# Kernel tuning notes

Hardware: AMD Instinct MI355X
Metric: run time of the kernel (lower is better)

## Reference

```python
import jax, jax.numpy as jnp
import numpy as np

B, T, C = 8, 1024, 768
H, D = 12, 64

def setup_inputs() -> dict:
    key = jax.random.key(0)
    ks = jax.random.split(key, 6)
    s = 0.02
    return {
        "x": jax.random.normal(ks[0], (B, T, C), dtype=jnp.float32),
        "Wq": jax.random.normal(ks[1], (H, C, D), dtype=jnp.float32) * s,
        "Wk": jax.random.normal(ks[2], (H, C, D), dtype=jnp.float32) * s,
        "Wv": jax.random.normal(ks[3], (H, C, D), dtype=jnp.float32) * s,
        "Wproj": jax.random.normal(ks[4], (C, C), dtype=jnp.float32) * s,
        "bproj": jnp.zeros((C,), dtype=jnp.float32),
    }

def reference(x, Wq, Wk, Wv, Wproj, bproj):
    # per-head projections, vectorized over heads: [B,H,T,D]
    q = jnp.einsum('btc,hcd->bhtd', x, Wq)
    k = jnp.einsum('btc,hcd->bhtd', x, Wk)
    v = jnp.einsum('btc,hcd->bhtd', x, Wv)
    scale = 1.0 / jnp.sqrt(jnp.asarray(q.shape[-1], q.dtype))
    scores = jnp.einsum('bhtd,bhsd->bhts', q, k) * scale  # [B,H,T,T]
    attn = jax.nn.softmax(scores, axis=-1)
    out = jnp.einsum('bhts,bhsd->bhtd', attn, v)          # [B,H,T,D]
    # concat heads along last dim -> [B,T,H*D]
    out = out.transpose(0, 2, 1, 3).reshape(x.shape[0], x.shape[1], -1)
    return out @ Wproj + bproj
```

## Files before the change

kernel.cpp:

```cpp
#include <hip/hip_runtime.h>
#include <hip/hip_bf16.h>

using u16 = unsigned short;

typedef __attribute__((ext_vector_type(8))) short bf16x8;
typedef __attribute__((ext_vector_type(4))) float f32x4;
typedef __attribute__((ext_vector_type(16))) float f32x16;

#define B_ 8
#define T_ 1024
#define C_ 768
#define H_ 12
#define D_ 64

typedef const void __attribute__((address_space(1))) gv_t;
typedef void __attribute__((address_space(3))) lv_t;

__device__ __forceinline__ void gload_lds16(const void* g, void* l) {
  __builtin_amdgcn_global_load_lds((gv_t*)g, (lv_t*)l, 16, 0, 0);
}

__device__ __forceinline__ u16 f2b(float f) {
  union { float f; unsigned u; } a; a.f = f;
  unsigned r = a.u + 0x7FFFu + ((a.u >> 16) & 1u);
  return (u16)(r >> 16);
}

__device__ __forceinline__ unsigned cvtpk_bf16(float lo, float hi) {
  unsigned r;
  asm("v_cvt_pk_bf16_f32 %0, %1, %2" : "=v"(r) : "v"(lo), "v"(hi));
  return r;
}
__device__ __forceinline__ void plane32_swap(unsigned &a, unsigned &b) {
  asm volatile("v_permlane32_swap_b32 %0, %1" : "+v"(a), "+v"(b));
}

__global__ __launch_bounds__(256) void cast_x(
    const float* __restrict__ in, u16* __restrict__ out)
{
  int i = (blockIdx.x * 256 + threadIdx.x) * 8;
  float4 a = *(const float4*)(in + i);
  float4 b = *(const float4*)(in + i + 4);
  union { bf16x8 v; u16 s[8]; } o;
  o.s[0] = f2b(a.x); o.s[1] = f2b(a.y); o.s[2] = f2b(a.z); o.s[3] = f2b(a.w);
  o.s[4] = f2b(b.x); o.s[5] = f2b(b.y); o.s[6] = f2b(b.z); o.s[7] = f2b(b.w);
  *(bf16x8*)(out + i) = o.v;
}

__global__ __launch_bounds__(256) void prep_weights(
    const float* __restrict__ Wq, const float* __restrict__ Wk,
    const float* __restrict__ Wv, const float* __restrict__ Wp,
    u16* __restrict__ Wqkvt, u16* __restrict__ Wpt)
{
  int idx = blockIdx.x * 256 + threadIdx.x;
  int p = idx / 589824;
  int r = idx - p * 589824;
  int n = r / 768, c = r - n * 768;
  if (p < 3) {
    const float* W = (p == 0) ? Wq : ((p == 1) ? Wk : Wv);
    int h = n >> 6, d = n & 63;
    Wqkvt[idx] = f2b(W[(size_t)h * (C_ * D_) + (size_t)c * D_ + d]);
  } else {
    Wpt[r] = f2b(Wp[(size_t)c * 768 + n]);
  }
}

#define GEMM_MAINLOOP(APTR, BPTR, KDIM)                                          \
  for (int k0 = 0; k0 < (KDIM); k0 += 64) {                                      \
    _Pragma("unroll")                                                            \
    for (int q = 0; q < 4; ++q) {                                                \
      int db = q * 4096 + t * 16;                                                \
      int row = db >> 7;                                                         \
      int cb = (db ^ ((row & 7) << 4)) & 127;                                    \
      gload_lds16((const char*)(APTR) + ((size_t)(m0 + row) * (KDIM) + k0) * 2 + cb, \
                  (char*)As + db);                                               \
      gload_lds16((const char*)(BPTR) + ((size_t)(n0 + row) * (KDIM) + k0) * 2 + cb, \
                  (char*)Bs + db);                                               \
    }                                                                            \
    asm volatile("s_waitcnt vmcnt(0)" ::: "memory");                             \
    __syncthreads();                                                             \
    _Pragma("unroll")                                                            \
    for (int kq = 0; kq < 2; ++kq) {                                             \
      bf16x8 af[4], bfr[4];                                                      \
      _Pragma("unroll")                                                          \
      for (int i = 0; i < 4; ++i) {                                              \
        int ra = wr + i * 16 + lr;                                               \
        int Ua = ra * 128 + kq * 64 + hc;                                        \
        af[i] = *(const bf16x8*)((const char*)As + (Ua ^ ((ra & 7) << 4)));      \
        int rb = wc + i * 16 + lr;                                               \
        int Ub = rb * 128 + kq * 64 + hc;                                        \
        bfr[i] = *(const bf16x8*)((const char*)Bs + (Ub ^ ((rb & 7) << 4)));     \
      }                                                                          \
      _Pragma("unroll")                                                          \
      for (int i = 0; i < 4; ++i)                                                \
        _Pragma("unroll")                                                        \
        for (int j = 0; j < 4; ++j)                                              \
          acc[i][j] = __builtin_amdgcn_mfma_f32_16x16x32_bf16(af[i], bfr[j],     \
                                                              acc[i][j], 0, 0, 0); \
    }                                                                            \
    __syncthreads();                                                             \
  }

__global__ __launch_bounds__(256) void gemm_qkv(
    const u16* __restrict__ X, const u16* __restrict__ Wt,
    u16* __restrict__ Qw, u16* __restrict__ Kw, u16* __restrict__ Vt)
{
  __shared__ __align__(16) u16 As[128 * 64];
  __shared__ __align__(16) u16 Bs[128 * 64];
  const int t = threadIdx.x;
  const int l = t & 63, w = t >> 6;
  const int lr = l & 15;
  const int hc = (l >> 4) * 16;
  const int m0 = blockIdx.x * 128;
  const int n0 = blockIdx.y * 128;
  const int wr = (w >> 1) * 64, wc = (w & 1) * 64;

  f32x4 acc[4][4] = {};
  GEMM_MAINLOOP(X, Wt, 768)

  #pragma unroll
  for (int j = 0; j < 4; ++j) {
    int col_g = n0 + wc + j * 16 + lr;
    int p = (col_g >= 1536) ? 2 : ((col_g >= 768) ? 1 : 0);
    int rr = col_g - p * 768;
    int h = rr >> 6, d = rr & 63;
    #pragma unroll
    for (int i = 0; i < 4; ++i) {
      int rg0 = m0 + wr + i * 16 + ((l >> 4) << 2);
      int b = rg0 >> 10, tt = rg0 & 1023;
      if (p == 0) {
        size_t base = (((size_t)b * H_ + h) * T_ + tt) * D_ + d;
        #pragma unroll
        for (int r = 0; r < 4; ++r)
          Qw[base + (size_t)r * D_] = f2b(acc[i][j][r] * 0.18033688f);
      } else if (p == 1) {
        size_t base = (((size_t)b * H_ + h) * T_ + tt) * D_ + d;
        #pragma unroll
        for (int r = 0; r < 4; ++r) Kw[base + (size_t)r * D_] = f2b(acc[i][j][r]);
      } else {
        unsigned long long pk =
            (unsigned long long)f2b(acc[i][j][0]) |
            ((unsigned long long)f2b(acc[i][j][1]) << 16) |
            ((unsigned long long)f2b(acc[i][j][2]) << 32) |
            ((unsigned long long)f2b(acc[i][j][3]) << 48);
        *reinterpret_cast<unsigned long long*>(
            &Vt[(((size_t)b * H_ + h) * D_ + d) * T_ + tt]) = pk;
      }
    }
  }
}

__global__ __launch_bounds__(256) void gemm_proj(
    const u16* __restrict__ A, const u16* __restrict__ Wt,
    const float* __restrict__ bias, float* __restrict__ O)
{
  __shared__ __align__(16) u16 As[128 * 64];
  __shared__ __align__(16) u16 Bs[128 * 64];
  const int t = threadIdx.x;
  const int l = t & 63, w = t >> 6;
  const int lr = l & 15;
  const int hc = (l >> 4) * 16;
  const int m0 = blockIdx.x * 128;
  const int n0 = blockIdx.y * 128;
  const int wr = (w >> 1) * 64, wc = (w & 1) * 64;

  f32x4 acc[4][4] = {};
  GEMM_MAINLOOP(A, Wt, 768)

  #pragma unroll
  for (int j = 0; j < 4; ++j) {
    int col_g = n0 + wc + j * 16 + lr;
    float bb = bias[col_g];
    #pragma unroll
    for (int i = 0; i < 4; ++i) {
      int rg0 = m0 + wr + i * 16 + ((l >> 4) << 2);
      #pragma unroll
      for (int r = 0; r < 4; ++r)
        O[(size_t)(rg0 + r) * C_ + col_g] = acc[i][j][r] + bb;
    }
  }
}

__global__ __launch_bounds__(256) void attn_fwd(
    const u16* __restrict__ Qw, const u16* __restrict__ Kw,
    const u16* __restrict__ VT, u16* __restrict__ AO)
{
  __shared__ __align__(16) u16 Ks[2][64 * 64];
  __shared__ __align__(16) u16 Vs[2][64 * 64];
  const int t = threadIdx.x, w = t >> 6, l = t & 63;
  const int lq = l & 31, lh = l >> 5;

  const int bid = blockIdx.x;
  const int bh = (bid & 7) * 12 + ((bid >> 3) >> 3);
  const int qt = (bid >> 3) & 7;
  const int b = bh / H_, h = bh - b * H_;
  const u16* Qh = Qw + (size_t)bh * (T_ * D_);
  const u16* Kh = Kw + (size_t)bh * (T_ * D_);
  const u16* Vh = VT + (size_t)bh * (D_ * T_);
  const int q0w = qt * 128 + w * 32;
  const int qrow = q0w + lq;

  bf16x8 qf[4];
  #pragma unroll
  for (int ks = 0; ks < 4; ++ks)
    qf[ks] = *(const bf16x8*)(Qh + (size_t)qrow * D_ + lh * 8 + ks * 16);

  f32x16 oA = {}, oB = {};
  float mrun = -1e30f, lrun = 0.f;

  const int db0 = t * 16, db1 = 4096 + t * 16;
  const int row0 = db0 >> 7, row1 = db1 >> 7;
  const int o20 = db0 & 127, o21 = db1 & 127;
  const int dsw0 = db0 ^ ((row0 & 7) << 4);
  const int dsw1 = db1 ^ ((row1 & 7) << 4);

  bf16x8 rk0, rk1, rv0, rv1;
  rk0 = *(const bf16x8*)((const char*)(Kh + (size_t)row0 * D_) + o20);
  rk1 = *(const bf16x8*)((const char*)(Kh + (size_t)row1 * D_) + o21);
  rv0 = *(const bf16x8*)((const char*)(Vh + (size_t)row0 * T_) + o20);
  rv1 = *(const bf16x8*)((const char*)(Vh + (size_t)row1 * T_) + o21);

  for (int kt_i = 0; kt_i < 16; ++kt_i) {
    const int cur = kt_i & 1;
    *(bf16x8*)((char*)Ks[cur] + dsw0) = rk0;
    *(bf16x8*)((char*)Ks[cur] + dsw1) = rk1;
    *(bf16x8*)((char*)Vs[cur] + dsw0) = rv0;
    *(bf16x8*)((char*)Vs[cur] + dsw1) = rv1;
    __syncthreads();

    if (kt_i < 15) {
      int kn = (kt_i + 1) * 64;
      rk0 = *(const bf16x8*)((const char*)(Kh + (size_t)(kn + row0) * D_) + o20);
      rk1 = *(const bf16x8*)((const char*)(Kh + (size_t)(kn + row1) * D_) + o21);
      rv0 = *(const bf16x8*)((const char*)(Vh + (size_t)row0 * T_ + kn) + o20);
      rv1 = *(const bf16x8*)((const char*)(Vh + (size_t)row1 * T_ + kn) + o21);
    }

    f32x16 sA = {}, sB = {};
    #pragma unroll
    for (int kvh = 0; kvh < 2; ++kvh) {
      bf16x8 ka[4];
      #pragma unroll
      for (int ks = 0; ks < 4; ++ks) {
        int row = lq + 32 * kvh;
        int U = row * 128 + ks * 32 + lh * 16;
        ka[ks] = *(const bf16x8*)((const char*)Ks[cur] + (U ^ ((row & 7) << 4)));
      }
      if (kvh == 0) {
        #pragma unroll
        for (int ks = 0; ks < 4; ++ks)
          sA = __builtin_amdgcn_mfma_f32_32x32x16_bf16(ka[ks], qf[ks], sA, 0, 0, 0);
      } else {
        #pragma unroll
        for (int ks = 0; ks < 4; ++ks)
          sB = __builtin_amdgcn_mfma_f32_32x32x16_bf16(ka[ks], qf[ks], sB, 0, 0, 0);
      }
    }

    float red[32];
    #pragma unroll
    for (int r = 0; r < 16; ++r) { red[r] = sA[r]; red[16 + r] = sB[r]; }
    #pragma unroll
    for (int stp = 16; stp > 0; stp >>= 1)
      #pragma unroll
      for (int r = 0; r < stp; ++r) red[r] = fmaxf(red[r], red[r + stp]);
    float mx = fmaxf(red[0], __shfl_xor(red[0], 32));
    float nm = fmaxf(mrun, mx);
    float alpha = exp2f(mrun - nm);
    mrun = nm;
    #pragma unroll
    for (int r = 0; r < 16; ++r) {
      sA[r] = exp2f(sA[r] - nm);
      sB[r] = exp2f(sB[r] - nm);
    }
    #pragma unroll
    for (int r = 0; r < 16; ++r) { red[r] = sA[r]; red[16 + r] = sB[r]; }
    #pragma unroll
    for (int stp = 16; stp > 0; stp >>= 1)
      #pragma unroll
      for (int r = 0; r < stp; ++r) red[r] += red[r + stp];
    float rs = red[0] + __shfl_xor(red[0], 32);
    lrun = lrun * alpha + rs;

    bf16x8 pb[4];
    #pragma unroll
    for (int ks = 0; ks < 4; ++ks) {
      f32x16& S = (ks < 2) ? sA : sB;
      const int g = (ks & 1) * 8;
      unsigned a0 = cvtpk_bf16(S[g + 0], S[g + 1]);
      unsigned a1 = cvtpk_bf16(S[g + 2], S[g + 3]);
      unsigned b0 = cvtpk_bf16(S[g + 4], S[g + 5]);
      unsigned b1 = cvtpk_bf16(S[g + 6], S[g + 7]);
      plane32_swap(a0, b0);
      plane32_swap(a1, b1);
      union { unsigned wd[4]; bf16x8 v; } u;
      u.wd[0] = a0; u.wd[1] = a1; u.wd[2] = b0; u.wd[3] = b1;
      pb[ks] = u.v;
    }

    #pragma unroll
    for (int r = 0; r < 16; ++r) { oA[r] *= alpha; oB[r] *= alpha; }

    #pragma unroll
    for (int dh = 0; dh < 2; ++dh) {
      bf16x8 va[4];
      #pragma unroll
      for (int ks = 0; ks < 4; ++ks) {
        int row = lq + 32 * dh;
        int U = row * 128 + ks * 32 + lh * 16;
        va[ks] = *(const bf16x8*)((const char*)Vs[cur] + (U ^ ((row & 7) << 4)));
      }
      if (dh == 0) {
        #pragma unroll
        for (int ks = 0; ks < 4; ++ks)
          oA = __builtin_amdgcn_mfma_f32_32x32x16_bf16(va[ks], pb[ks], oA, 0, 0, 0);
      } else {
        #pragma unroll
        for (int ks = 0; ks < 4; ++ks)
          oB = __builtin_amdgcn_mfma_f32_32x32x16_bf16(va[ks], pb[ks], oB, 0, 0, 0);
      }
    }
  }

  float inv = 1.0f / lrun;
  size_t base = ((size_t)b * T_ + qrow) * C_ + h * D_;
  #pragma unroll
  for (int dh = 0; dh < 2; ++dh) {
    const f32x16& OO = dh ? oB : oA;
    #pragma unroll
    for (int g = 0; g < 4; ++g) {
      int d0 = 8 * g + 4 * lh + 32 * dh;
      unsigned long long pk =
          (unsigned long long)f2b(OO[4 * g + 0] * inv) |
          ((unsigned long long)f2b(OO[4 * g + 1] * inv) << 16) |
          ((unsigned long long)f2b(OO[4 * g + 2] * inv) << 32) |
          ((unsigned long long)f2b(OO[4 * g + 3] * inv) << 48);
      *reinterpret_cast<unsigned long long*>(&AO[base + d0]) = pk;
    }
  }
}

extern "C" void kernel_launch(void* const* d_in, const int* in_sizes, int n_in,
                              void* d_out, int out_size, void* d_ws, size_t ws_size,
                              hipStream_t stream) {
  (void)in_sizes; (void)n_in; (void)out_size;
  const float* x     = (const float*)d_in[0];
  const float* Wq    = (const float*)d_in[1];
  const float* Wk    = (const float*)d_in[2];
  const float* Wv    = (const float*)d_in[3];
  const float* Wproj = (const float*)d_in[4];
  const float* bproj = (const float*)d_in[5];

  const size_t NEEDED = 55050240;
  if (ws_size < NEEDED) return;

  char* ws = (char*)d_ws;
  u16* Wpt   = (u16*)(ws);
  u16* Qw    = (u16*)(ws + 1179648);
  u16* Kw    = (u16*)(ws + 13762560);
  u16* Vt    = (u16*)(ws + 26345472);
  u16* Xb    = (u16*)(ws + 38928384);
  u16* AO    = (u16*)(ws + 38928384);
  u16* Wqkvt = (u16*)(ws + 51511296);

  cast_x<<<dim3(3072), dim3(256), 0, stream>>>(x, Xb);
  prep_weights<<<dim3(9216), dim3(256), 0, stream>>>(Wq, Wk, Wv, Wproj, Wqkvt, Wpt);
  gemm_qkv<<<dim3(64, 18), dim3(256), 0, stream>>>(Xb, Wqkvt, Qw, Kw, Vt);
  attn_fwd<<<dim3(768), dim3(256), 0, stream>>>(Qw, Kw, Vt, AO);
  gemm_proj<<<dim3(64, 6), dim3(256), 0, stream>>>(AO, Wpt, bproj, (float*)d_out);
}
```

Baseline: 151.9 us.

## Fuse prep kernels, async LDS loads in attention, lazy softmax rescale

Merges the x cast and weight-prep kernels into a single launch to save one kernel launch. In attention, K/V tiles now go straight to LDS through global_load_lds and are prefetched into the other buffer, replacing the register-staged copy. The online softmax first combines sA and sB element-wise to shorten the max/sum reductions, and rescales the running max and output only when the new max exceeds the old one by more than 8 (log2 units), skipping that multiply most of the time. The lazy rescale keeps results exact in principle but lets exp2 values grow up to 2^8 before renormalising, so bf16 P values carry a larger range.

```diff
diff --git a/kernel.cpp b/kernel.cpp
--- a/kernel.cpp
+++ b/kernel.cpp
@@ -35,33 +35,33 @@
   asm volatile("v_permlane32_swap_b32 %0, %1" : "+v"(a), "+v"(b));
 }
 
-__global__ __launch_bounds__(256) void cast_x(
-    const float* __restrict__ in, u16* __restrict__ out)
-{
-  int i = (blockIdx.x * 256 + threadIdx.x) * 8;
-  float4 a = *(const float4*)(in + i);
-  float4 b = *(const float4*)(in + i + 4);
-  union { bf16x8 v; u16 s[8]; } o;
-  o.s[0] = f2b(a.x); o.s[1] = f2b(a.y); o.s[2] = f2b(a.z); o.s[3] = f2b(a.w);
-  o.s[4] = f2b(b.x); o.s[5] = f2b(b.y); o.s[6] = f2b(b.z); o.s[7] = f2b(b.w);
-  *(bf16x8*)(out + i) = o.v;
-}
-
-__global__ __launch_bounds__(256) void prep_weights(
+__global__ __launch_bounds__(256) void prep_all(
+    const float* __restrict__ x,
     const float* __restrict__ Wq, const float* __restrict__ Wk,
     const float* __restrict__ Wv, const float* __restrict__ Wp,
-    u16* __restrict__ Wqkvt, u16* __restrict__ Wpt)
+    u16* __restrict__ Xb, u16* __restrict__ Wqkvt, u16* __restrict__ Wpt)
 {
-  int idx = blockIdx.x * 256 + threadIdx.x;
-  int p = idx / 589824;
-  int r = idx - p * 589824;
-  int n = r / 768, c = r - n * 768;
-  if (p < 3) {
-    const float* W = (p == 0) ? Wq : ((p == 1) ? Wk : Wv);
-    int h = n >> 6, d = n & 63;
-    Wqkvt[idx] = f2b(W[(size_t)h * (C_ * D_) + (size_t)c * D_ + d]);
+  int bb = blockIdx.x;
+  if (bb < 3072) {
+    int i = (bb * 256 + threadIdx.x) * 8;
+    float4 a = *(const float4*)(x + i);
+    float4 b = *(const float4*)(x + i + 4);
+    union { bf16x8 v; u16 s[8]; } o;
+    o.s[0] = f2b(a.x); o.s[1] = f2b(a.y); o.s[2] = f2b(a.z); o.s[3] = f2b(a.w);
+    o.s[4] = f2b(b.x); o.s[5] = f2b(b.y); o.s[6] = f2b(b.z); o.s[7] = f2b(b.w);
+    *(bf16x8*)(Xb + i) = o.v;
   } else {
-    Wpt[r] = f2b(Wp[(size_t)c * 768 + n]);
+    int idx = (bb - 3072) * 256 + threadIdx.x;
+    int p = idx / 589824;
+    int r = idx - p * 589824;
+    int n = r / 768, c = r - n * 768;
+    if (p < 3) {
+      const float* W = (p == 0) ? Wq : ((p == 1) ? Wk : Wv);
+      int h = n >> 6, d = n & 63;
+      Wqkvt[idx] = f2b(W[(size_t)h * (C_ * D_) + (size_t)c * D_ + d]);
+    } else {
+      Wpt[r] = f2b(Wp[(size_t)c * 768 + n]);
+    }
   }
 }
 
@@ -195,8 +195,8 @@
   const int qt = (bid >> 3) & 7;
   const int b = bh / H_, h = bh - b * H_;
   const u16* Qh = Qw + (size_t)bh * (T_ * D_);
-  const u16* Kh = Kw + (size_t)bh * (T_ * D_);
-  const u16* Vh = VT + (size_t)bh * (D_ * T_);
+  const char* Kp = (const char*)(Kw + (size_t)bh * (T_ * D_));
+  const char* Vp = (const char*)(VT + (size_t)bh * (D_ * T_));
   const int q0w = qt * 128 + w * 32;
   const int qrow = q0w + lq;
 
@@ -210,77 +210,76 @@
 
   const int db0 = t * 16, db1 = 4096 + t * 16;
   const int row0 = db0 >> 7, row1 = db1 >> 7;
-  const int o20 = db0 & 127, o21 = db1 & 127;
-  const int dsw0 = db0 ^ ((row0 & 7) << 4);
-  const int dsw1 = db1 ^ ((row1 & 7) << 4);
-
-  bf16x8 rk0, rk1, rv0, rv1;
-  rk0 = *(const bf16x8*)((const char*)(Kh + (size_t)row0 * D_) + o20);
-  rk1 = *(const bf16x8*)((const char*)(Kh + (size_t)row1 * D_) + o21);
-  rv0 = *(const bf16x8*)((const char*)(Vh + (size_t)row0 * T_) + o20);
-  rv1 = *(const bf16x8*)((const char*)(Vh + (size_t)row1 * T_) + o21);
+  const int cb0 = (db0 ^ ((row0 & 7) << 4)) & 127;
+  const int cb1 = (db1 ^ ((row1 & 7) << 4)) & 127;
+
+#define ISSUE_TILE(KT, BUF)                                                     \
+  gload_lds16(Kp + (size_t)((KT) + row0) * 128 + cb0, (char*)Ks[BUF] + db0);    \
+  gload_lds16(Kp + (size_t)((KT) + row1) * 128 + cb1, (char*)Ks[BUF] + db1);    \
+  gload_lds16(Vp + (size_t)row0 * 2048 + (KT) * 2 + cb0, (char*)Vs[BUF] + db0); \
+  gload_lds16(Vp + (size_t)row1 * 2048 + (KT) * 2 + cb1, (char*)Vs[BUF] + db1);
+
+  ISSUE_TILE(0, 0)
 
   for (int kt_i = 0; kt_i < 16; ++kt_i) {
     const int cur = kt_i & 1;
-    *(bf16x8*)((char*)Ks[cur] + dsw0) = rk0;
-    *(bf16x8*)((char*)Ks[cur] + dsw1) = rk1;
-    *(bf16x8*)((char*)Vs[cur] + dsw0) = rv0;
-    *(bf16x8*)((char*)Vs[cur] + dsw1) = rv1;
+    asm volatile("s_waitcnt vmcnt(0)" ::: "memory");
     __syncthreads();
-
-    if (kt_i < 15) {
-      int kn = (kt_i + 1) * 64;
-      rk0 = *(const bf16x8*)((const char*)(Kh + (size_t)(kn + row0) * D_) + o20);
-      rk1 = *(const bf16x8*)((const char*)(Kh + (size_t)(kn + row1) * D_) + o21);
-      rv0 = *(const bf16x8*)((const char*)(Vh + (size_t)row0 * T_ + kn) + o20);
-      rv1 = *(const bf16x8*)((const char*)(Vh + (size_t)row1 * T_ + kn) + o21);
-    }
+    if (kt_i < 15) { ISSUE_TILE((kt_i + 1) * 64, cur ^ 1) }
 
     f32x16 sA = {}, sB = {};
-    #pragma unroll
-    for (int kvh = 0; kvh < 2; ++kvh) {
+    {
       bf16x8 ka[4];
       #pragma unroll
       for (int ks = 0; ks < 4; ++ks) {
-        int row = lq + 32 * kvh;
+        int row = lq;
         int U = row * 128 + ks * 32 + lh * 16;
         ka[ks] = *(const bf16x8*)((const char*)Ks[cur] + (U ^ ((row & 7) << 4)));
       }
-      if (kvh == 0) {
-        #pragma unroll
-        for (int ks = 0; ks < 4; ++ks)
-          sA = __builtin_amdgcn_mfma_f32_32x32x16_bf16(ka[ks], qf[ks], sA, 0, 0, 0);
-      } else {
-        #pragma unroll
-        for (int ks = 0; ks < 4; ++ks)
-          sB = __builtin_amdgcn_mfma_f32_32x32x16_bf16(ka[ks], qf[ks], sB, 0, 0, 0);
-      }
-    }
-
-    float red[32];
-    #pragma unroll
-    for (int r = 0; r < 16; ++r) { red[r] = sA[r]; red[16 + r] = sB[r]; }
-    #pragma unroll
-    for (int stp = 16; stp > 0; stp >>= 1)
-      #pragma unroll
-      for (int r = 0; r < stp; ++r) red[r] = fmaxf(red[r], red[r + stp]);
-    float mx = fmaxf(red[0], __shfl_xor(red[0], 32));
-    float nm = fmaxf(mrun, mx);
-    float alpha = exp2f(mrun - nm);
-    mrun = nm;
-    #pragma unroll
-    for (int r = 0; r < 16; ++r) {
-      sA[r] = exp2f(sA[r] - nm);
-      sB[r] = exp2f(sB[r] - nm);
-    }
-    #pragma unroll
-    for (int r = 0; r < 16; ++r) { red[r] = sA[r]; red[16 + r] = sB[r]; }
-    #pragma unroll
-    for (int stp = 16; stp > 0; stp >>= 1)
-      #pragma unroll
-      for (int r = 0; r < stp; ++r) red[r] += red[r + stp];
-    float rs = red[0] + __shfl_xor(red[0], 32);
-    lrun = lrun * alpha + rs;
+      #pragma unroll
+      for (int ks = 0; ks < 4; ++ks)
+        sA = __builtin_amdgcn_mfma_f32_32x32x16_bf16(ka[ks], qf[ks], sA, 0, 0, 0);
+      #pragma unroll
+      for (int ks = 0; ks < 4; ++ks) {
+        int row = lq + 32;
+        int U = row * 128 + ks * 32 + lh * 16;
+        ka[ks] = *(const bf16x8*)((const char*)Ks[cur] + (U ^ ((row & 7) << 4)));
+      }
+      #pragma unroll
+      for (int ks = 0; ks < 4; ++ks)
+        sB = __builtin_amdgcn_mfma_f32_32x32x16_bf16(ka[ks], qf[ks], sB, 0, 0, 0);
+    }
+
+    {
+      float a16[16];
+      #pragma unroll
+      for (int r = 0; r < 16; ++r) a16[r] = fmaxf(sA[r], sB[r]);
+      #pragma unroll
+      for (int stp = 8; stp > 0; stp >>= 1)
+        #pragma unroll
+        for (int r = 0; r < stp; ++r) a16[r] = fmaxf(a16[r], a16[r + stp]);
+      float mx = fmaxf(a16[0], __shfl_xor(a16[0], 32));
+      if (!__all(mx <= mrun + 8.0f)) {
+        float nm = fmaxf(mrun, mx);
+        float alpha = exp2f(mrun - nm);
+        mrun = nm;
+        lrun *= alpha;
+        #pragma unroll
+        for (int r = 0; r < 16; ++r) { oA[r] *= alpha; oB[r] *= alpha; }
+      }
+      #pragma unroll
+      for (int r = 0; r < 16; ++r) {
+        sA[r] = exp2f(sA[r] - mrun);
+        sB[r] = exp2f(sB[r] - mrun);
+      }
+      #pragma unroll
+      for (int r = 0; r < 16; ++r) a16[r] = sA[r] + sB[r];
+      #pragma unroll
+      for (int stp = 8; stp > 0; stp >>= 1)
+        #pragma unroll
+        for (int r = 0; r < stp; ++r) a16[r] += a16[r + stp];
+      lrun += a16[0] + __shfl_xor(a16[0], 32);
+    }
 
     bf16x8 pb[4];
     #pragma unroll
@@ -298,29 +297,29 @@
       pb[ks] = u.v;
     }
 
-    #pragma unroll
-    for (int r = 0; r < 16; ++r) { oA[r] *= alpha; oB[r] *= alpha; }
-
-    #pragma unroll
-    for (int dh = 0; dh < 2; ++dh) {
+    {
       bf16x8 va[4];
       #pragma unroll
       for (int ks = 0; ks < 4; ++ks) {
-        int row = lq + 32 * dh;
+        int row = lq;
         int U = row * 128 + ks * 32 + lh * 16;
         va[ks] = *(const bf16x8*)((const char*)Vs[cur] + (U ^ ((row & 7) << 4)));
       }
-      if (dh == 0) {
-        #pragma unroll
-        for (int ks = 0; ks < 4; ++ks)
-          oA = __builtin_amdgcn_mfma_f32_32x32x16_bf16(va[ks], pb[ks], oA, 0, 0, 0);
-      } else {
-        #pragma unroll
-        for (int ks = 0; ks < 4; ++ks)
-          oB = __builtin_amdgcn_mfma_f32_32x32x16_bf16(va[ks], pb[ks], oB, 0, 0, 0);
-      }
-    }
-  }
+      #pragma unroll
+      for (int ks = 0; ks < 4; ++ks)
+        oA = __builtin_amdgcn_mfma_f32_32x32x16_bf16(va[ks], pb[ks], oA, 0, 0, 0);
+      #pragma unroll
+      for (int ks = 0; ks < 4; ++ks) {
+        int row = lq + 32;
+        int U = row * 128 + ks * 32 + lh * 16;
+        va[ks] = *(const bf16x8*)((const char*)Vs[cur] + (U ^ ((row & 7) << 4)));
+      }
+      #pragma unroll
+      for (int ks = 0; ks < 4; ++ks)
+        oB = __builtin_amdgcn_mfma_f32_32x32x16_bf16(va[ks], pb[ks], oB, 0, 0, 0);
+    }
+  }
+#undef ISSUE_TILE
 
   float inv = 1.0f / lrun;
   size_t base = ((size_t)b * T_ + qrow) * C_ + h * D_;
@@ -363,8 +362,7 @@
   u16* AO    = (u16*)(ws + 38928384);
   u16* Wqkvt = (u16*)(ws + 51511296);
 
-  cast_x<<<dim3(3072), dim3(256), 0, stream>>>(x, Xb);
-  prep_weights<<<dim3(9216), dim3(256), 0, stream>>>(Wq, Wk, Wv, Wproj, Wqkvt, Wpt);
+  prep_all<<<dim3(12288), dim3(256), 0, stream>>>(x, Wq, Wk, Wv, Wproj, Xb, Wqkvt, Wpt);
   gemm_qkv<<<dim3(64, 18), dim3(256), 0, stream>>>(Xb, Wqkvt, Qw, Kw, Vt);
   attn_fwd<<<dim3(768), dim3(256), 0, stream>>>(Qw, Kw, Vt, AO);
   gemm_proj<<<dim3(64, 6), dim3(256), 0, stream>>>(AO, Wpt, bproj, (float*)d_out);
```

New measurement: 151.1 us. No clear change (-0.5%).
